# Performance work log

Hardware: AMD Instinct MI355X
Metric: run time of the kernel (lower is better)

Reference implementation:

```python
import jax, jax.numpy as jnp
import numpy as np
from jax import lax

F32 = jnp.float32
EDT_ITERS = 16  # iterations for erosion-based distance transform approximation


def _maxpool(x, win):
    # x: (B, 1, D, H, W); stride-1 'SAME' max pool (pads with -inf like torch)
    return lax.reduce_window(x, -jnp.inf, lax.max, (1, 1) + win, (1, 1, 1, 1, 1), 'SAME')


def _minpool(x, win):
    return -_maxpool(-x, win)


def soft_erode(img):
    p1 = _minpool(img, (3, 1, 1))
    p2 = _minpool(img, (1, 3, 1))
    p3 = _minpool(img, (1, 1, 3))
    return jnp.minimum(jnp.minimum(p1, p2), p3)


def soft_dilate(img):
    return _maxpool(img, (3, 3, 3))


def soft_open(img):
    return soft_dilate(soft_erode(img))


def soft_skel(img, num_iter=10):
    # clDice soft skeletonization (SoftSkeletonize, num_iter=10)
    skel = jax.nn.relu(img - soft_open(img))
    for _ in range(num_iter):
        img = soft_erode(img)
        delta = jax.nn.relu(img - soft_open(img))
        skel = skel + jax.nn.relu(delta - skel * delta)
    return skel


def edt_approx(mask):
    # mask: (B, D, H, W) binary float. Distance-to-background via iterated
    # 3x3x3 erosion (chessboard metric approximation of distance_transform_edt).
    m = mask[:, None]

    def body(carry, _):
        cur, acc = carry
        acc = acc + cur
        cur = _minpool(cur, (3, 3, 3))
        return (cur, acc), None

    (_, acc), _ = lax.scan(body, (m, jnp.zeros_like(m)), None, length=EDT_ITERS)
    return acc[:, 0]


def get_weights(mask_input, skel_input, prob_flag):
    # dim == 3 path of the original get_weights, vectorized over batch
    if prob_flag:
        mask = (mask_input > 0.5).astype(F32)
        skel = (skel_input > 0.5).astype(F32)
    else:
        mask, skel = mask_input, skel_input
    dist = lax.stop_gradient(edt_approx(mask)) * mask
    skel_radius = dist * skel
    red = (1, 2, 3)
    rmax = jnp.maximum(jnp.max(skel_radius, axis=red, keepdims=True), 1.0)
    rmin = jnp.maximum(jnp.min(skel_radius, axis=red, keepdims=True), 1.0)
    dist_map_norm = jnp.minimum(dist, rmax) / rmax
    skel_R_norm = skel_radius / rmax
    I_norm = ((rmax - skel_radius + rmin) / rmax) ** 2 * skel  # dim == 3 -> squared
    if prob_flag:
        return dist_map_norm * mask_input, skel_R_norm * mask_input, I_norm * skel_input
    return dist_map_norm * mask, skel_R_norm * mask, I_norm * skel


def binary_fg_prob(net_output):
    # max over foreground channels, 2-way softmax, foreground probability
    fore = jnp.max(net_output[:, 1:], axis=1, keepdims=True)
    logits2 = jnp.concatenate([net_output[:, :1], fore], axis=1)
    return jax.nn.softmax(logits2, axis=1)[:, 1]  # (B, D, H, W)


def general_union(pred, tgt, weight):
    smooth, alpha, eps = 1.0, 0.1, 1e-4
    inter = jnp.sum(weight * (pred + eps) ** 0.7 * tgt)
    union = jnp.sum(weight * (alpha * pred + (1.0 - alpha) * tgt))
    return 1.0 - (inter + smooth) / (union + smooth)


def union_loss(net_output, target):
    prob = binary_fg_prob(net_output)
    y_true = (target[:, 0] > 0).astype(F32)
    hard = lax.stop_gradient((prob > 0.5).astype(F32))
    skel_pred_hard = lax.stop_gradient(soft_skel(hard[:, None], 10)[:, 0])
    skel_true = lax.stop_gradient(soft_skel(y_true[:, None], 10)[:, 0])
    skel_pred_prob = skel_pred_hard * prob
    q_vl, _, q_sl = get_weights(y_true, skel_true, prob_flag=False)
    q_vp, _, q_sp = get_weights(prob, skel_pred_prob, prob_flag=True)
    return general_union(q_sp, q_vl, q_sp) + general_union(q_vp, q_sl, q_sl)


def cldice_loss(net_output, target, num_iter=10, smooth=1.0):
    prob = binary_fg_prob(net_output)
    y_true = (target[:, 0] > 0).astype(F32)
    skel_pred = soft_skel(prob[:, None], num_iter)[:, 0]
    skel_true = soft_skel(y_true[:, None], num_iter)[:, 0]
    tprec = (jnp.sum(skel_pred * y_true) + smooth) / (jnp.sum(skel_pred) + smooth)
    tsens = (jnp.sum(skel_true * prob) + smooth) / (jnp.sum(skel_true) + smooth)
    return 1.0 - 2.0 * tprec * tsens / (tprec + tsens)


def soft_dice_loss(net_output, target, smooth=1e-5):
    # nnUNet SoftDiceLoss: softmax nonlin, batch_dice=True, do_bg=False
    pred = jax.nn.softmax(net_output, axis=1)
    C = net_output.shape[1]
    onehot = jnp.moveaxis(jax.nn.one_hot(target[:, 0], C, dtype=F32), -1, 1)
    axes = (0, 2, 3, 4)
    tp = jnp.sum(pred * onehot, axis=axes)
    fp = jnp.sum(pred * (1.0 - onehot), axis=axes)
    fn = jnp.sum((1.0 - pred) * onehot, axis=axes)
    dc = (2.0 * tp + smooth) / (2.0 * tp + fp + fn + smooth)
    return -jnp.mean(dc[1:])


def ce_loss(net_output, labels):
    logp = jax.nn.log_softmax(net_output, axis=1)
    nll = -jnp.take_along_axis(logp, labels[:, None], axis=1)[:, 0]
    return jnp.mean(nll)


def _sobel_kernels():
    sx = np.array([[-1, 0, 1], [-2, 0, 2], [-1, 0, 1]], np.float32)
    kx_t = np.stack([sx, sx, sx], axis=0)[None, None]  # (1,1,3,3,3) OIDHW
    ky_t = np.transpose(kx_t, (0, 1, 3, 2, 4))
    kz_t = np.transpose(kx_t, (0, 1, 4, 2, 3))

    def pred_k(k):  # (1,2,3,3,3): second input channel is all-zero like the torch kernel
        return np.concatenate([k, np.zeros_like(k)], axis=1)

    return (pred_k(kx_t), pred_k(ky_t), pred_k(kz_t)), (kx_t, ky_t, kz_t)


def _conv3d(x, k):
    return lax.conv_general_dilated(x, jnp.asarray(k), (1, 1, 1), 'SAME',
                                    dimension_numbers=('NCDHW', 'OIDHW', 'NCDHW'))


def directional_loss(pred, target):
    kp, kt = _sobel_kernels()
    gp = jnp.stack([_conv3d(pred, k) for k in kp], axis=-1)    # (B,1,D,H,W,3)
    gt = jnp.stack([_conv3d(target, k) for k in kt], axis=-1)  # (B,1,D,H,W,3)

    def normalize(v):
        n = jnp.linalg.norm(v, axis=-1, keepdims=True)
        return v / jnp.maximum(n, 1e-12)

    gpn, gtn = normalize(gp), normalize(gt)
    num = jnp.sum(gpn * gtn, axis=-1)
    den = jnp.maximum(jnp.linalg.norm(gpn, axis=-1) * jnp.linalg.norm(gtn, axis=-1), 1e-8)
    return 1.0 - jnp.mean(num / den)


def connectivity_loss(pred, target):
    pb = (pred > 0.5).astype(F32)
    tb = (target > 0.5).astype(F32)
    return jnp.mean(jnp.abs(pb - tb))  # broadcasts (B,2,...) against (B,1,...)


def combined_loss(net_output, target):
    tgt_f = target.astype(F32)
    labels = target[:, 0]
    return (soft_dice_loss(net_output, target)
            + ce_loss(net_output, labels)
            + cldice_loss(net_output, target)
            + directional_loss(net_output, tgt_f)
            + connectivity_loss(net_output, tgt_f)
            + union_loss(net_output, target))


def setup_inputs() -> dict:
    key = jax.random.key(0)
    k1, k2 = jax.random.split(key)
    net_output = jax.random.normal(k1, (2, 2, 64, 128, 128), dtype=jnp.float32)
    target = jax.random.randint(k2, (2, 1, 64, 128, 128), 0, 2, dtype=jnp.int32)
    return {'net_output': net_output, 'target': target, 't_skeletonize_flage': 0}


def reference(net_output, target, t_skeletonize_flage):
    # t_skeletonize_flage=0 -> soft (morphological) skeletonization path
    return combined_loss(net_output, target)
```

## Files before the change

kernel.cpp:

```cpp
#include <hip/hip_runtime.h>
#include <math.h>

typedef unsigned long long u64;
typedef unsigned int u32;
typedef unsigned short u16;
typedef unsigned char u8;

#define VOL 1048576
#define NTOT 2097152
#define NWORDS 32768
#define PC0 2048
#define PC1 2048

union HU { u16 u; _Float16 h; };
__device__ __forceinline__ float h2f(u16 u){ HU x; x.u=u; return (float)x.h; }
__device__ __forceinline__ u16 f2h(float f){ HU x; x.h=(_Float16)f; return x.u; }
#define H_ONE2 0x3C003C00u

__device__ __forceinline__ u32 pmin(u32 a, u32 b){ u32 r; asm("v_pk_min_f16 %0, %1, %2" : "=v"(r) : "v"(a), "v"(b)); return r; }
__device__ __forceinline__ u32 pmax(u32 a, u32 b){ u32 r; asm("v_pk_max_f16 %0, %1, %2" : "=v"(r) : "v"(a), "v"(b)); return r; }

__device__ __forceinline__ double wred(double v){
  #pragma unroll
  for(int o=32;o;o>>=1) v += __shfl_down(v, o);
// ... 13 lines not shown
  u64 win;
  if (a<0)        win = w0 << (-a);
  else if (a==0)  win = w0;
  else if (a<64)  win = (w0>>a)|(w1<<(64-a));
  else            win = w1>>(a-64);
  if (x<31) win |= (1ull<<(31-x))-1;
  if (x>95) win |= (~0ull)<<(159-x);
  u64 inv = ~win;
  u64 tl = inv & 0xFFFFFFFFull;
  u64 tr = inv>>31;
  int dl = tl ? (31-(63-__clzll(tl))) : 99;
  int dr = tr ? (__ffsll((unsigned long long)tr)-1) : 99;
  return min(min(dl,dr),16);
}

__global__ __launch_bounds__(256) void k_init(const float* __restrict__ net, const int* __restrict__ tgt,
    u16* __restrict__ img, u16* __restrict__ prob, u64* __restrict__ ybits, u64* __restrict__ hbits,
    u64* __restrict__ bimg2, u8* __restrict__ dA, double* __restrict__ part)
{
  __shared__ u64 nyb[32], nhb[32];
  __shared__ u64 swy[16], swh[16];
  __shared__ double sw[5][4];
  int tid = threadIdx.x;
  int r = blockIdx.x*256 + tid;
  int n0 = r<<2;
  int b = n0>>20, v0 = n0&(VOL-1);
  const float* nb = net + (size_t)b*(2*VOL);
  float4 a0 = *(const float4*)&nb[v0];
  float4 a1 = *(const float4*)&nb[VOL+v0];
  int4  tv = *(const int4*)&tgt[n0];
  float x0a[4] = {a0.x,a0.y,a0.z,a0.w};
  float x1a[4] = {a1.x,a1.y,a1.z,a1.w};
  int   ta[4]  = {tv.x,tv.y,tv.z,tv.w};
  double ce=0,tp=0,spr=0,sy=0,conn=0;
  u32 pk[2] = {0,0};
  u32 y4=0, h4=0;
  #pragma unroll
  for(int e=0;e<4;e++){
    float d = x1a[e]-x0a[e];
    int yb = (ta[e]>0) ? 1 : 0;
    float p = 1.f/(1.f+__expf(-d));
    y4 |= (u32)yb<<e;
    h4 |= (u32)(d>0.f)<<e;
    pk[e>>1] |= (u32)f2h(p) << ((e&1)*16);
    ce += (double)(log1pf(__expf(-fabsf(d))) + fmaxf(yb? -d : d, 0.f));
    tp += (double)p*yb;
    spr += (double)p;
    sy += (double)yb;
    conn += (double)((int)((x0a[e]>0.5f)!=(yb!=0)) + (int)((x1a[e]>0.5f)!=(yb!=0)));
  }
  u32* f1 = (u32*)img;
  u32* f4 = (u32*)prob;
  int pi = r<<1;
  f1[pi] = pk[0]; f1[pi+1] = pk[1];
  f4[pi] = pk[0]; f4[pi+1] = pk[1];
  ((u8*)nyb)[tid] = (u8)y4;
  ((u8*)nhb)[tid] = (u8)h4;
  __syncthreads();
  if (tid < 16){
    u64 wy = (u64)nib_compact(nyb[tid*2]) | ((u64)nib_compact(nyb[tid*2+1])<<32);
    u64 wh = (u64)nib_compact(nhb[tid*2]) | ((u64)nib_compact(nhb[tid*2+1])<<32);
    int wi = blockIdx.x*16 + tid;
    ybits[wi]=wy; bimg2[wi]=wy;
    hbits[wi]=wh; bimg2[NWORDS+wi]=wh;
    swy[tid]=wy; swh[tid]=wh;
  }
  __syncthreads();
  {
    int ln = tid<<2;
    int row = ln>>7;
    int xq = ln&127;
    int gn0 = blockIdx.x*1024 + ln;
    u64 wy0 = swy[row*2], wy1 = swy[row*2+1];
    u64 wh0 = swh[row*2], wh1 = swh[row*2+1];
    u32 oy4=0, oh4=0;
    #pragma unroll
    for(int e=0;e<4;e++){
      oy4 |= (u32)edt_x1(wy0,wy1,xq+e) << (8*e);
      oh4 |= (u32)edt_x1(wh0,wh1,xq+e) << (8*e);
    }
    *(u32*)&dA[gn0] = oy4;
    *(u32*)&dA[(size_t)NTOT+gn0] = oh4;
  }
  int wid = tid>>6, lane = tid&63;
  double vals[5] = {ce,tp,spr,sy,conn};
  #pragma unroll
  for(int s=0;s<5;s++){ double rr = wred(vals[s]); if(lane==0) sw[s][wid]=rr; }
  __syncthreads();
  if(tid==0){
    #pragma unroll
    for(int s=0;s<5;s++) part[(size_t)s*PC0 + blockIdx.x] = sw[s][0]+sw[s][1]+sw[s][2]+sw[s][3];
  }
}

template<bool INIT>
__global__ __launch_bounds__(512) void fskel2(const u16* __restrict__ imgin, u16* __restrict__ imgout,
                                              u16* __restrict__ skel)
{
  __shared__ u32 A_[3920];
  __shared__ u32 B_[2592];
  __shared__ u32 C_[1800];
  int bid = blockIdx.x;
  int xb = bid&3, yb=(bid>>2)&15, zb=(bid>>6)&7, b=bid>>9;
  int X0=xb*32, Y0=yb*8, Z0=zb*8;
  const u32* vin = (const u32*)(imgin + (size_t)b*VOL);
  u32* vout = (u32*)(imgout + (size_t)b*VOL);
  u32* skl = (u32*)(skel + (size_t)b*VOL);
  int tid = threadIdx.x;

  for (int idx=tid; idx<3920; idx+=512){
    int z = idx/280; int rem = idx - z*280; int y = rem/20; int px = rem - y*20;
    int gz = Z0-3+z, gy = Y0-3+y, gx = X0-4+2*px;
    bool ok = ((unsigned)gz<64u) & ((unsigned)gy<128u) & ((unsigned)gx<128u);
    A_[idx] = ok ? vin[(gz<<13)+(gy<<6)+(gx>>1)] : H_ONE2;
  }
  __syncthreads();
  for (int idx=tid; idx<2592; idx+=512){
    int z = idx/216; int rem = idx - z*216; int y = rem/18; int px = rem - y*18;
    int gz = Z0-2+z, gy = Y0-2+y;
    bool zok = (unsigned)gz<64u, yok = (unsigned)gy<128u;
    bool xout = ((X0==0)&&(px==0)) || ((X0==96)&&(px==17));
    u32 v = H_ONE2;
    if (zok && yok && !xout){
      int c = (z+1)*280 + (y+1)*20 + (px+1);
      u32 C0=A_[c], L=A_[c-1], R=A_[c+1];
      u32 SL=(L>>16)|(C0<<16), SR=(C0>>16)|(R<<16);
      u32 m = pmin(pmin(SL,SR), C0);
      m = pmin(m, pmin(A_[c-20],A_[c+20]));
      v = pmin(m, pmin(A_[c-280],A_[c+280]));
    }
    B_[idx] = v;
  }
  __syncthreads();
  for (int idx=tid; idx<1800; idx+=512){
    int z = idx/180; int rem = idx - z*180; int y = rem/18; int px = rem - y*18;
    int gz = Z0-1+z, gy = Y0-1+y;
    bool zok=(unsigned)gz<64u, yok=(unsigned)gy<128u;
    bool xout = ((X0==0)&&(px==0)) || ((X0==96)&&(px==17));
    int pxm = (px>0)?px-1:0, pxp=(px<17)?px+1:17;
    u32 v = 0;
    if (zok && yok && !xout){
      int c = (z+1)*216 + (y+1)*18;
      u32 C0=B_[c+px], L=B_[c+pxm], R=B_[c+pxp];
      u32 SL=(L>>16)|(C0<<16), SR=(C0>>16)|(R<<16);
      u32 m = pmin(pmin(SL,SR), C0);
      m = pmin(m, pmin(B_[c+px-18],B_[c+px+18]));
      v = pmin(m, pmin(B_[c-216+px],B_[c+216+px]));
    }
    C_[idx] = v;
    if (px>=1 && px<=16 && y>=1 && y<=8 && z>=1 && z<=8)
      vout[(gz<<13)+(gy<<6)+((X0-2+2*px)>>1)] = v;
  }
  int zq = tid>>7, cc = tid&127;
  int oy = cc>>4, opx = cc&15;
  u32 ek0[2], ek1[2];
  #pragma unroll
  for(int j=0;j<2;j++){
    int z = zq*2+j;
    ek0[j] = A_[(z+3)*280 + (oy+3)*20 + (opx+2)];
    ek1[j] = B_[(z+2)*216 + (oy+2)*18 + (opx+1)];
  }
  __syncthreads();
  u32* X1 = A_; u32* X2 = A_ + 1600;
  for (int idx=tid; idx<3200; idx+=512){
    int arr = (idx>=1600);
    int r2 = arr ? idx-1600 : idx;
    int z = r2/160; int rem = r2 - z*160; int y = rem>>4; int px = rem&15;
    u32 v;
    if (!arr){
      int gz = Z0-1+z, gy = Y0-1+y;
      bool ok = ((unsigned)gz<64u) && ((unsigned)gy<128u);
      int c = (z+1)*216 + (y+1)*18 + (px+1);
      u32 C0=B_[c], L=B_[c-1], R=B_[c+1];
      if ((X0==0)&&(px==0)) L=0;
      if ((X0==96)&&(px==15)) R=0;
      u32 SL=(L>>16)|(C0<<16), SR=(C0>>16)|(R<<16);
      v = pmax(pmax(SL,SR), C0);
      if (!ok) v = 0;
    } else {
      int c = z*180 + y*18 + (px+1);
      u32 C0=C_[c], L=C_[c-1], R=C_[c+1];
      u32 SL=(L>>16)|(C0<<16), SR=(C0>>16)|(R<<16);
      v = pmax(pmax(SL,SR), C0);
    }
    A_[idx] = v;
  }
  __syncthreads();
  for (int idx=tid; idx<2560; idx+=512){
    int arr = (idx>=1280);
    int r2 = arr ? idx-1280 : idx;
    int z = r2>>7; int rem = r2&127; int y = rem>>4; int px = rem&15;
    const u32* Xs = arr ? X2 : X1;
    int c = z*160 + y*16 + px;
    B_[idx] = pmax(pmax(Xs[c], Xs[c+16]), Xs[c+32]);
  }
  __syncthreads();
  u32* Y1 = B_; u32* Y2 = B_ + 1280;
  {
    int gx = X0 + 2*opx;
    #pragma unroll
    for(int j=0;j<2;j++){
      int z = zq*2+j;
      int gz = Z0+z;
      int c = z*128 + oy*16 + opx;
      u32 o1 = pmax(pmax(Y1[c], Y1[c+128]), Y1[c+256]);
      u32 o2 = pmax(pmax(Y2[c], Y2[c+128]), Y2[c+256]);
      u32 idx = (u32)((gz<<13) + ((Y0+oy)<<6) + (gx>>1));
      float d0l = fmaxf(h2f((u16)ek0[j]) - h2f((u16)o1), 0.f);
      float d0h = fmaxf(h2f((u16)(ek0[j]>>16)) - h2f((u16)(o1>>16)), 0.f);
      float d1l = fmaxf(h2f((u16)ek1[j]) - h2f((u16)o2), 0.f);
      float d1h = fmaxf(h2f((u16)(ek1[j]>>16)) - h2f((u16)(o2>>16)), 0.f);
      float sl_, sh_;
      if (INIT){ sl_ = d0l; sh_ = d0h; }
      else {
        u32 swv = skl[idx];
        sl_ = h2f((u16)swv); sh_ = h2f((u16)(swv>>16));
        sl_ += fmaxf(d0l - sl_*d0l, 0.f); sh_ += fmaxf(d0h - sh_*d0h, 0.f);
      }
      sl_ += fmaxf(d1l - sl_*d1l, 0.f); sh_ += fmaxf(d1h - sh_*d1h, 0.f);
      skl[idx] = (u32)f2h(sl_) | ((u32)f2h(sh_)<<16);
    }
  }
}

__global__ __launch_bounds__(512) void fskel1(const u16* __restrict__ imgin, u16* __restrict__ skel)
{
  __shared__ u32 A2[2880];
  __shared__ u32 B2[1800];
  int bid = blockIdx.x;
  int xb = bid&3, yb=(bid>>2)&15, zb=(bid>>6)&7, b=bid>>9;
  int X0=xb*32, Y0=yb*8, Z0=zb*8;
  const u32* vin = (const u32*)(imgin + (size_t)b*VOL);
  u32* skl = (u32*)(skel + (size_t)b*VOL);
  int tid = threadIdx.x;
  for (int idx=tid; idx<2880; idx+=512){
    int z = idx/240; int rem = idx - z*240; int y = rem/20; int px = rem - y*20;
    int gz = Z0-2+z, gy = Y0-2+y, gx = X0-4+2*px;
    bool ok = ((unsigned)gz<64u) & ((unsigned)gy<128u) & ((unsigned)gx<128u);
    A2[idx] = ok ? vin[(gz<<13)+(gy<<6)+(gx>>1)] : H_ONE2;
  }
  __syncthreads();
  for (int idx=tid; idx<1800; idx+=512){
    int z = idx/180; int rem = idx - z*180; int y = rem/18; int px = rem - y*18;
    int gz = Z0-1+z, gy = Y0-1+y;
    bool zok=(unsigned)gz<64u, yok=(unsigned)gy<128u;
    bool xout = ((X0==0)&&(px==0)) || ((X0==96)&&(px==17));
    int pxm = (px>0)?px-1:0, pxp=(px<17)?px+1:17;
    u32 v = 0;
    if (zok && yok && !xout){
      int c = (z+1)*240 + (y+1)*20;
      u32 C0=A2[c+px+1], L=A2[c+pxm+1], R=A2[c+pxp+1];
      u32 SL=(L>>16)|(C0<<16), SR=(C0>>16)|(R<<16);
      u32 m = pmin(pmin(SL,SR), C0);
      m = pmin(m, pmin(A2[c+px+1-20],A2[c+px+1+20]));
      v = pmin(m, pmin(A2[c-240+px+1],A2[c+240+px+1]));
    }
    B2[idx] = v;
  }
  int zq = tid>>7, cc = tid&127;
  int oy = cc>>4, opx = cc&15;
  u32 ek[2];
  #pragma unroll
  for(int j=0;j<2;j++){
    int z = zq*2+j;
    ek[j] = A2[(z+2)*240 + (oy+2)*20 + (opx+2)];
  }
  __syncthreads();
  u32* X = A2;
  for (int idx=tid; idx<1600; idx+=512){
    int z = idx/160; int rem = idx - z*160; int y = rem>>4; int px = rem&15;
    int c = z*180 + y*18 + (px+1);
    u32 C0=B2[c], L=B2[c-1], R=B2[c+1];
    u32 SL=(L>>16)|(C0<<16), SR=(C0>>16)|(R<<16);
    A2[idx] = pmax(pmax(SL,SR), C0);
  }
  __syncthreads();
  u32* Y = B2;
  for (int idx=tid; idx<1280; idx+=512){
    int z = idx>>7; int rem = idx&127; int y = rem>>4; int px = rem&15;
    int c = z*160 + y*16 + px;
    B2[idx] = pmax(pmax(X[c], X[c+16]), X[c+32]);
  }
  __syncthreads();
  {
    int gx = X0 + 2*opx;
    #pragma unroll
    for(int j=0;j<2;j++){
      int z = zq*2+j;
      int gz = Z0+z;
      int c = z*128 + oy*16 + opx;
      u32 o = pmax(pmax(Y[c], Y[c+128]), Y[c+256]);
      u32 idx = (u32)((gz<<13) + ((Y0+oy)<<6) + (gx>>1));
      float dl = fmaxf(h2f((u16)ek[j]) - h2f((u16)o), 0.f);
      float dh = fmaxf(h2f((u16)(ek[j]>>16)) - h2f((u16)(o>>16)), 0.f);
      u32 swv = skl[idx];
      float sl_ = h2f((u16)swv), sh_ = h2f((u16)(swv>>16));
      sl_ += fmaxf(dl - sl_*dl, 0.f); sh_ += fmaxf(dh - sh_*dh, 0.f);
      skl[idx] = (u32)f2h(sl_) | ((u32)f2h(sh_)<<16);
    }
  }
}

__device__ __forceinline__ u64 berode_x(const u64* P, int tid){
  u64 c = P[tid];
  if (tid & 1) return c & ((c<<1)|(P[tid-1]>>63)) & ((c>>1)|(1ull<<63));
  else         return c & ((c<<1)|1ull) & ((c>>1)|(P[tid+1]<<63));
}
__device__ __forceinline__ u64 bdilate_x(const u64* P, int tid){
  u64 c = P[tid];
  if (tid & 1) return c | (c<<1) | (P[tid-1]>>63) | (c>>1);
  else         return c | (c<<1) | (c>>1) | (P[tid+1]<<63);
}

template<bool INIT>
__global__ __launch_bounds__(256) void bskel(const u64* __restrict__ imgin, u64* __restrict__ imgout,
                                             u64* __restrict__ skel)
{
  __shared__ u64 simg[4][256];
  __shared__ u64 se1[6][256];
  __shared__ u64 se2[2][256];
  __shared__ u64 sM[4][256];
  int bid = blockIdx.x;
  int tzb = bid & 31, b = (bid>>5)&1, m = bid>>6;
  int z0 = tzb*2, z1 = z0+2;
  size_t base = (size_t)m*NWORDS + (size_t)b*16384;
  const u64* vin = imgin + base;
  u64* vout = imgout + base;
  u64* skl = skel + base;
  int tid = threadIdx.x;
  int y = tid>>1;

  for (int s = z0-3; s <= z1+6; ++s){
    if (s <= z1+2)
      simg[(s+96)&3][tid] = ((unsigned)s<64u) ? vin[(s<<8)+tid] : ~0ull;
    { int t = s-2;
      if (t >= z0-2 && t <= z1+1){
        u64 r = ~0ull;
        if ((unsigned)t<64u){
          const u64* P = simg[(t+96)&3];
          if (INIT) r = P[tid];
          else {
            r = berode_x(P, tid);
            if(y>0)   r &= P[tid-2];
            if(y<127) r &= P[tid+2];
// ... 6 lines not shown
    { int t = s-4;
      if (t >= z0-1 && t <= z1){
        u64 r = 0;
        if ((unsigned)t<64u){
          const u64* P = se1[(t+96)%6];
          r = berode_x(P, tid);
          if(y>0)   r &= P[tid-2];
          if(y<127) r &= P[tid+2];
          r &= se1[(t-1+96)%6][tid] & se1[(t+1+96)%6][tid];
        }
        se2[(t+96)&1][tid] = r;
      }
    }
    { int t = s-5;
      if (t >= z0-1 && t <= z1){
        const u64* P = se2[(t+96)&1];
        u64 dm = bdilate_x(P, tid);
        if(y>0)   dm |= bdilate_x(P, tid-2);
        if(y<127) dm |= bdilate_x(P, tid+2);
        sM[(t+96)&3][tid] = dm;
      }
    }
    { int z = s-7;
      if (z >= z0 && z < z1){
        u64 open_ = sM[(z-1+96)&3][tid] | sM[(z+96)&3][tid] | sM[(z+1+96)&3][tid];
        u64 e1v = se1[(z+96)%6][tid];
        u64 d = e1v & ~open_;
        int gw = (z<<8)+tid;
        if (INIT) skl[gw] = d;
        else { skl[gw] |= d; vout[gw] = e1v; }
      }
    }
    __syncthreads();
  }
}

__global__ __launch_bounds__(256) void edt_py(const u8* __restrict__ din, u8* __restrict__ dout){
  int g = blockIdx.x*256 + threadIdx.x;
  int n = g & (NTOT-1);
  int c = (n >> 7) & 127;
  size_t idx = (size_t)g;
  int best = din[idx];
  #pragma unroll 4
  for (int k=1; k<=16; ++k){
    if (best <= k) break;
    int v = 255;
    if (c-k >= 0)   v = din[idx - (size_t)k*128];
    if (c+k < 128)  v = min(v, (int)din[idx + (size_t)k*128]);
    best = min(best, max(k, v));
  }
  dout[idx] = (u8)best;
}

__global__ __launch_bounds__(256) void edt_pz_part(const u8* __restrict__ din, u8* __restrict__ dout,
    const u64* __restrict__ skel2, const u64* __restrict__ hbits,
    u8* __restrict__ pmaxv, u8* __restrict__ pminv)
{
  int tid = threadIdx.x;
  int g = blockIdx.x*256 + tid;
  int m = g >> 21;
  int n = g & (NTOT-1);
  int c = (n >> 14) & 63;
  size_t idx = (size_t)g;
  int best = din[idx];
  #pragma unroll 4
  for (int k=1; k<=16; ++k){
// ... 93 lines not shown
    }
    wrow[tid] = wn;
  }
  __syncthreads();
  for (int idx=tid; idx<1920; idx+=256){
    int zr = idx/320; int rem = idx-zr*320; int yr = rem>>5; int x = rem&31;
    int c = zr*340 + yr*34 + x;
    float l0=lp[c], l1=lp[c+1], l2=lp[c+2];
    dxp[idx] = l2-l0;
    sxp[idx] = l0+2.f*l1+l2;
    u64 wn = wrow[zr*10+yr];
    int bm=(int)((wn>>x)&1ull), b1=(int)((wn>>(x+1))&1ull), bp=(int)((wn>>(x+2))&1ull);
    dxt8[idx] = (char)(bp-bm);
    sxt8[idx] = (u8)(bm+2*b1+bp);
  }
  __syncthreads();
  int oy = tid>>5, ox = tid&31;
  float A1[6],A2[6],A3[6];
  int   B1v[6],B2v[6],B3v[6];
  #pragma unroll
  for(int zr=0; zr<6; ++zr){
    int base = zr*320 + oy*32 + ox;
    float d0=dxp[base], d1=dxp[base+32], d2=dxp[base+64];
    A1[zr] = d0+2.f*d1+d2;
    A2[zr] = d0+d1+d2;
    float s0=sxp[base], s1=sxp[base+32], s2=sxp[base+64];
    A3[zr] = s0+s1+s2;
    int t0=dxt8[base], t1=dxt8[base+32], t2=dxt8[base+64];
    B1v[zr] = t0+2*t1+t2;
    B2v[zr] = t0+t1+t2;
    int u0=sxt8[base], u1=sxt8[base+32], u2=sxt8[base+64];
    B3v[zr] = u0+u1+u2;
  }
  double fsob=0,cl1=0,cl2=0,cl3=0,cl4=0,i1=0,un1=0,i2=0,un2=0;
  #pragma unroll
  for(int zc=0; zc<4; ++zc){
    float gpx = A1[zc]+A1[zc+1]+A1[zc+2];
    float gpy = A2[zc]+2.f*A2[zc+1]+A2[zc+2];
    float gpz = A3[zc+2]-A3[zc];
    float ftx = (float)(B1v[zc]+B1v[zc+1]+B1v[zc+2]);
    float fty = (float)(B2v[zc]+2*B2v[zc+1]+B2v[zc+2]);
    float ftz = (float)(B3v[zc+2]-B3v[zc]);
    float s1 = gpx*gpx+gpy*gpy+gpz*gpz;
    float s2 = ftx*ftx+fty*fty+ftz*ftz;
    if (s1>0.f && s2>0.f){
      float ip = rsqrtf(s1), it = rsqrtf(s2);
      fsob += (double)((gpx*ftx+gpy*fty+gpz*ftz)*ip*it);
    }
    int gz=Z0+zc, gy=Y0+oy, gx=X0+ox;
    int n = (b<<20)+(gz<<14)+(gy<<7)+gx;
    int yb = (int)((wrow[(zc+1)*10+(oy+1)] >> (ox+1)) & 1ull);
    int wi = n>>6, bit = n&63;
    int hd = (int)((hbits[wi]>>bit)&1ull);
    int sT = (int)((skel2[wi]>>bit)&1ull);
    int sH = (int)((skel2[NWORDS+wi]>>bit)&1ull);
    float dT = (float)acc[n];
    float dH = (float)acc[(size_t)NTOT+n];
    float p  = h2f(prob[n]);
    float sk = h2f(skelp[n]);
    cl1 += (double)(sk*(float)yb);
    cl2 += (double)sk;
    float q_vl = yb ? fminf(dT,rmaxT)/rmaxT : 0.f;
    if (sT){
      cl3 += (double)p; cl4 += 1.0;
      float t=(rmaxT-dT+rminT)/rmaxT; float q_sl=t*t;
      float q_vp = fminf(dH,rmaxH)/rmaxH*p;
      i2  += (double)(q_sl*__powf(q_vp+1e-4f,0.7f)*q_sl);
      un2 += (double)(q_sl*(0.1f*q_vp+0.9f*q_sl));
    }
    if (sH & hd){
      float t=(rmaxH-dH+rminH)/rmaxH; float q_sp=t*t*p;
      i1  += (double)(q_sp*__powf(q_sp+1e-4f,0.7f)*q_vl);
      un1 += (double)(q_sp*(0.1f*q_sp+0.9f*q_vl));
    }
  }
  int wid = tid>>6, lane = tid&63;
  double vals[9] = {fsob,cl1,cl2,cl3,cl4,i1,un1,i2,un2};
  #pragma unroll
  for(int s=0;s<9;s++){ double rr = wred(vals[s]); if(lane==0) sw[s][wid]=rr; }
  __syncthreads();
  if(tid==0){
    #pragma unroll
    for(int s=0;s<9;s++) part1[(size_t)s*PC1 + bid] = sw[s][0]+sw[s][1]+sw[s][2]+sw[s][3];
  }
}

__global__ __launch_bounds__(256) void k_reduce_mid(const double* __restrict__ part0,
                                                    const double* __restrict__ part1,
                                                    double* __restrict__ tot){
  int s = blockIdx.x;
  const double* src; int n;
  if (s < 5){ src = part0 + (size_t)s*PC0; n = PC0; }
  else      { src = part1 + (size_t)(s-5)*PC1; n = PC1; }
  double v=0;
  for(int i=threadIdx.x;i<n;i+=256) v += src[i];
  __shared__ double sd[256];
  sd[threadIdx.x]=v; __syncthreads();
  for(int k=128;k>0;k>>=1){ if((int)threadIdx.x<k) sd[threadIdx.x]+=sd[threadIdx.x+k]; __syncthreads(); }
  if(threadIdx.x==0) tot[s]=sd[0];
}

__global__ void k_fin(const double* __restrict__ tot, float* __restrict__ out){
  if(threadIdx.x==0 && blockIdx.x==0){
    const double N = (double)NTOT;
    double ce = tot[0]/N;
    double tp=tot[1], fp=tot[2]-tot[1], fn=tot[3]-tot[1];
    double dice = -((2.0*tp+1e-5)/(2.0*tp+fp+fn+1e-5));
    double conn = tot[4]/(2.0*N);
    double dir  = 1.0 - tot[5]/N;
    double tprec = (tot[6]+1.0)/(tot[7]+1.0);
// ... 6 lines not shown
}

extern "C" void kernel_launch(void* const* d_in, const int* in_sizes, int n_in,
                              void* d_out, int out_size, void* d_ws, size_t ws_size,
                              hipStream_t stream)
{
  (void)in_sizes; (void)n_in; (void)out_size; (void)ws_size;
  const float* net = (const float*)d_in[0];
  const int*   tgt = (const int*)d_in[1];
  float* out = (float*)d_out;
  char* w = (char*)d_ws;
  const size_t MB = 1024*1024;
  u16* F1 = (u16*)(w + 0*MB);
  u16* F2 = (u16*)(w + 4*MB);
  u16* F3 = (u16*)(w + 8*MB);
  u16* F4 = (u16*)(w + 12*MB);
  u64* ybits = (u64*)(w + 16*MB);
  u64* hbits = ybits + NWORDS;
  u64* skel2 = hbits + NWORDS;
  u64* bping = skel2 + 2*NWORDS;
  u64* bpong = bping + 2*NWORDS;
  u8*  dA    = (u8*)(bpong + 2*NWORDS);
  u8*  dB    = dA + (size_t)2*NTOT;
  double* part0 = (double*)(dB + (size_t)2*NTOT);
  double* part1 = part0 + (size_t)5*PC0;
  double* tot   = part1 + (size_t)9*PC1;
  u8* pmaxv = (u8*)(tot + 16);
  u8* pminv = pmaxv + 16384;
  u32* mm  = (u32*)(pminv + 16384);

  k_init<<<PC0, 256, 0, stream>>>(net, tgt, F1, F4, ybits, hbits, bping, dA, part0);

  bskel<true><<<128,256,0,stream>>>(bping, bpong, skel2);
  {
    u64* pi=bping; u64* po=bpong;
    for(int i=0;i<10;i++){ bskel<false><<<128,256,0,stream>>>(pi,po,skel2); u64* t=pi; pi=po; po=t; }
  }

  fskel2<true><<<1024,512,0,stream>>>(F1, F3, F2);
  fskel2<false><<<1024,512,0,stream>>>(F3, F1, F2);
  fskel2<false><<<1024,512,0,stream>>>(F1, F3, F2);
  fskel2<false><<<1024,512,0,stream>>>(F3, F1, F2);
  fskel2<false><<<1024,512,0,stream>>>(F1, F3, F2);
  fskel1<<<1024,512,0,stream>>>(F3, F2);

  const int GE = (2*NTOT)/256;
  edt_py<<<GE,256,0,stream>>>(dA, dB);
  edt_pz_part<<<GE,256,0,stream>>>(dB, dA, skel2, hbits, pmaxv, pminv);
  rmm2<<<1,256,0,stream>>>(pmaxv, pminv, mm);

  k_tail<<<PC1,256,0,stream>>>(net, F4, F2, ybits, hbits, skel2, dA, mm, part1);
  k_reduce_mid<<<14,256,0,stream>>>(part0, part1, tot);
  k_fin<<<1,64,0,stream>>>(tot, out);
}
```

Baseline: 303.2 us.

## Fuse binary skeleton iterations into float skeleton kernels as extra blocks

Six of the ten binary-skeleton iterations now run as 128 extra blocks appended to each float soft-skeleton launch, in a combined fsk_b kernel that dispatches on block index. The binary work uses a z-streaming erode/open pipeline over bit-packed words, so six small, poorly occupied launches disappear and that work overlaps with the float tiles. Per-thread loss accumulators in k_init and k_tail also switch from double to float, with double kept only for the cross-lane reduction. This trades some accumulation precision and a larger shared-memory footprint per block for fewer launches and fewer fp64 operations.

```diff
diff --git a/kernel.cpp b/kernel.cpp
--- a/kernel.cpp
+++ b/kernel.cpp
@@ -69,7 +69,7 @@
   float x0a[4] = {a0.x,a0.y,a0.z,a0.w};
   float x1a[4] = {a1.x,a1.y,a1.z,a1.w};
   int   ta[4]  = {tv.x,tv.y,tv.z,tv.w};
-  double ce=0,tp=0,spr=0,sy=0,conn=0;
+  float ce=0,tp=0,spr=0,sy=0,conn=0;
   u32 pk[2] = {0,0};
   u32 y4=0, h4=0;
   #pragma unroll
@@ -80,11 +80,11 @@
     y4 |= (u32)yb<<e;
     h4 |= (u32)(d>0.f)<<e;
     pk[e>>1] |= (u32)f2h(p) << ((e&1)*16);
-    ce += (double)(log1pf(__expf(-fabsf(d))) + fmaxf(yb? -d : d, 0.f));
-    tp += (double)p*yb;
-    spr += (double)p;
-    sy += (double)yb;
-    conn += (double)((int)((x0a[e]>0.5f)!=(yb!=0)) + (int)((x1a[e]>0.5f)!=(yb!=0)));
+    ce += log1pf(__expf(-fabsf(d))) + fmaxf(yb? -d : d, 0.f);
+    tp += p*(float)yb;
+    spr += p;
+    sy += (float)yb;
+    conn += (float)((int)((x0a[e]>0.5f)!=(yb!=0)) + (int)((x1a[e]>0.5f)!=(yb!=0)));
   }
   u32* f1 = (u32*)img;
   u32* f4 = (u32*)prob;
@@ -120,7 +120,7 @@
     *(u32*)&dA[(size_t)NTOT+gn0] = oh4;
   }
   int wid = tid>>6, lane = tid&63;
-  double vals[5] = {ce,tp,spr,sy,conn};
+  double vals[5] = {(double)ce,(double)tp,(double)spr,(double)sy,(double)conn};
   #pragma unroll
   for(int s=0;s<5;s++){ double rr = wred(vals[s]); if(lane==0) sw[s][wid]=rr; }
   __syncthreads();
@@ -130,223 +130,15 @@
   }
 }
 
-template<bool INIT>
-__global__ __launch_bounds__(512) void fskel2(const u16* __restrict__ imgin, u16* __restrict__ imgout,
-                                              u16* __restrict__ skel)
-{
-  __shared__ u32 A_[3920];
-  __shared__ u32 B_[2592];
-  __shared__ u32 C_[1800];
-  int bid = blockIdx.x;
-  int xb = bid&3, yb=(bid>>2)&15, zb=(bid>>6)&7, b=bid>>9;
-  int X0=xb*32, Y0=yb*8, Z0=zb*8;
-  const u32* vin = (const u32*)(imgin + (size_t)b*VOL);
-  u32* vout = (u32*)(imgout + (size_t)b*VOL);
-  u32* skl = (u32*)(skel + (size_t)b*VOL);
-  int tid = threadIdx.x;
-
-  for (int idx=tid; idx<3920; idx+=512){
-    int z = idx/280; int rem = idx - z*280; int y = rem/20; int px = rem - y*20;
-    int gz = Z0-3+z, gy = Y0-3+y, gx = X0-4+2*px;
-    bool ok = ((unsigned)gz<64u) & ((unsigned)gy<128u) & ((unsigned)gx<128u);
-    A_[idx] = ok ? vin[(gz<<13)+(gy<<6)+(gx>>1)] : H_ONE2;
-  }
-  __syncthreads();
-  for (int idx=tid; idx<2592; idx+=512){
-    int z = idx/216; int rem = idx - z*216; int y = rem/18; int px = rem - y*18;
-    int gz = Z0-2+z, gy = Y0-2+y;
-    bool zok = (unsigned)gz<64u, yok = (unsigned)gy<128u;
-    bool xout = ((X0==0)&&(px==0)) || ((X0==96)&&(px==17));
-    u32 v = H_ONE2;
-    if (zok && yok && !xout){
-      int c = (z+1)*280 + (y+1)*20 + (px+1);
-      u32 C0=A_[c], L=A_[c-1], R=A_[c+1];
-      u32 SL=(L>>16)|(C0<<16), SR=(C0>>16)|(R<<16);
-      u32 m = pmin(pmin(SL,SR), C0);
-      m = pmin(m, pmin(A_[c-20],A_[c+20]));
-      v = pmin(m, pmin(A_[c-280],A_[c+280]));
-    }
-    B_[idx] = v;
-  }
-  __syncthreads();
-  for (int idx=tid; idx<1800; idx+=512){
-    int z = idx/180; int rem = idx - z*180; int y = rem/18; int px = rem - y*18;
-    int gz = Z0-1+z, gy = Y0-1+y;
-    bool zok=(unsigned)gz<64u, yok=(unsigned)gy<128u;
-    bool xout = ((X0==0)&&(px==0)) || ((X0==96)&&(px==17));
-    int pxm = (px>0)?px-1:0, pxp=(px<17)?px+1:17;
-    u32 v = 0;
-    if (zok && yok && !xout){
-      int c = (z+1)*216 + (y+1)*18;
-      u32 C0=B_[c+px], L=B_[c+pxm], R=B_[c+pxp];
-      u32 SL=(L>>16)|(C0<<16), SR=(C0>>16)|(R<<16);
-      u32 m = pmin(pmin(SL,SR), C0);
-      m = pmin(m, pmin(B_[c+px-18],B_[c+px+18]));
-      v = pmin(m, pmin(B_[c-216+px],B_[c+216+px]));
-    }
-    C_[idx] = v;
-    if (px>=1 && px<=16 && y>=1 && y<=8 && z>=1 && z<=8)
-      vout[(gz<<13)+(gy<<6)+((X0-2+2*px)>>1)] = v;
-  }
-  int zq = tid>>7, cc = tid&127;
-  int oy = cc>>4, opx = cc&15;
-  u32 ek0[2], ek1[2];
-  #pragma unroll
-  for(int j=0;j<2;j++){
-    int z = zq*2+j;
-    ek0[j] = A_[(z+3)*280 + (oy+3)*20 + (opx+2)];
-    ek1[j] = B_[(z+2)*216 + (oy+2)*18 + (opx+1)];
-  }
-  __syncthreads();
-  u32* X1 = A_; u32* X2 = A_ + 1600;
-  for (int idx=tid; idx<3200; idx+=512){
-    int arr = (idx>=1600);
-    int r2 = arr ? idx-1600 : idx;
-    int z = r2/160; int rem = r2 - z*160; int y = rem>>4; int px = rem&15;
-    u32 v;
-    if (!arr){
-      int gz = Z0-1+z, gy = Y0-1+y;
-      bool ok = ((unsigned)gz<64u) && ((unsigned)gy<128u);
-      int c = (z+1)*216 + (y+1)*18 + (px+1);
-      u32 C0=B_[c], L=B_[c-1], R=B_[c+1];
-      if ((X0==0)&&(px==0)) L=0;
-      if ((X0==96)&&(px==15)) R=0;
-      u32 SL=(L>>16)|(C0<<16), SR=(C0>>16)|(R<<16);
-      v = pmax(pmax(SL,SR), C0);
-      if (!ok) v = 0;
-    } else {
-      int c = z*180 + y*18 + (px+1);
-      u32 C0=C_[c], L=C_[c-1], R=C_[c+1];
-      u32 SL=(L>>16)|(C0<<16), SR=(C0>>16)|(R<<16);
-      v = pmax(pmax(SL,SR), C0);
-    }
-    A_[idx] = v;
-  }
-  __syncthreads();
-  for (int idx=tid; idx<2560; idx+=512){
-    int arr = (idx>=1280);
-    int r2 = arr ? idx-1280 : idx;
-    int z = r2>>7; int rem = r2&127; int y = rem>>4; int px = rem&15;
-    const u32* Xs = arr ? X2 : X1;
-    int c = z*160 + y*16 + px;
-    B_[idx] = pmax(pmax(Xs[c], Xs[c+16]), Xs[c+32]);
-  }
-  __syncthreads();
-  u32* Y1 = B_; u32* Y2 = B_ + 1280;
-  {
-    int gx = X0 + 2*opx;
-    #pragma unroll
-    for(int j=0;j<2;j++){
-      int z = zq*2+j;
-      int gz = Z0+z;
-      int c = z*128 + oy*16 + opx;
-      u32 o1 = pmax(pmax(Y1[c], Y1[c+128]), Y1[c+256]);
-      u32 o2 = pmax(pmax(Y2[c], Y2[c+128]), Y2[c+256]);
-      u32 idx = (u32)((gz<<13) + ((Y0+oy)<<6) + (gx>>1));
-      float d0l = fmaxf(h2f((u16)ek0[j]) - h2f((u16)o1), 0.f);
-      float d0h = fmaxf(h2f((u16)(ek0[j]>>16)) - h2f((u16)(o1>>16)), 0.f);
-      float d1l = fmaxf(h2f((u16)ek1[j]) - h2f((u16)o2), 0.f);
-      float d1h = fmaxf(h2f((u16)(ek1[j]>>16)) - h2f((u16)(o2>>16)), 0.f);
-      float sl_, sh_;
-      if (INIT){ sl_ = d0l; sh_ = d0h; }
-      else {
-        u32 swv = skl[idx];
-        sl_ = h2f((u16)swv); sh_ = h2f((u16)(swv>>16));
-        sl_ += fmaxf(d0l - sl_*d0l, 0.f); sh_ += fmaxf(d0h - sh_*d0h, 0.f);
-      }
-      sl_ += fmaxf(d1l - sl_*d1l, 0.f); sh_ += fmaxf(d1h - sh_*d1h, 0.f);
-      skl[idx] = (u32)f2h(sl_) | ((u32)f2h(sh_)<<16);
-    }
-  }
-}
-
-__global__ __launch_bounds__(512) void fskel1(const u16* __restrict__ imgin, u16* __restrict__ skel)
-{
-  __shared__ u32 A2[2880];
-  __shared__ u32 B2[1800];
-  int bid = blockIdx.x;
-  int xb = bid&3, yb=(bid>>2)&15, zb=(bid>>6)&7, b=bid>>9;
-  int X0=xb*32, Y0=yb*8, Z0=zb*8;
-  const u32* vin = (const u32*)(imgin + (size_t)b*VOL);
-  u32* skl = (u32*)(skel + (size_t)b*VOL);
-  int tid = threadIdx.x;
-  for (int idx=tid; idx<2880; idx+=512){
-    int z = idx/240; int rem = idx - z*240; int y = rem/20; int px = rem - y*20;
-    int gz = Z0-2+z, gy = Y0-2+y, gx = X0-4+2*px;
-    bool ok = ((unsigned)gz<64u) & ((unsigned)gy<128u) & ((unsigned)gx<128u);
-    A2[idx] = ok ? vin[(gz<<13)+(gy<<6)+(gx>>1)] : H_ONE2;
-  }
-  __syncthreads();
-  for (int idx=tid; idx<1800; idx+=512){
-    int z = idx/180; int rem = idx - z*180; int y = rem/18; int px = rem - y*18;
-    int gz = Z0-1+z, gy = Y0-1+y;
-    bool zok=(unsigned)gz<64u, yok=(unsigned)gy<128u;
-    bool xout = ((X0==0)&&(px==0)) || ((X0==96)&&(px==17));
-    int pxm = (px>0)?px-1:0, pxp=(px<17)?px+1:17;
-    u32 v = 0;
-    if (zok && yok && !xout){
-      int c = (z+1)*240 + (y+1)*20;
-      u32 C0=A2[c+px+1], L=A2[c+pxm+1], R=A2[c+pxp+1];
-      u32 SL=(L>>16)|(C0<<16), SR=(C0>>16)|(R<<16);
-      u32 m = pmin(pmin(SL,SR), C0);
-      m = pmin(m, pmin(A2[c+px+1-20],A2[c+px+1+20]));
-      v = pmin(m, pmin(A2[c-240+px+1],A2[c+240+px+1]));
-    }
-    B2[idx] = v;
-  }
-  int zq = tid>>7, cc = tid&127;
-  int oy = cc>>4, opx = cc&15;
-  u32 ek[2];
-  #pragma unroll
-  for(int j=0;j<2;j++){
-    int z = zq*2+j;
-    ek[j] = A2[(z+2)*240 + (oy+2)*20 + (opx+2)];
-  }
-  __syncthreads();
-  u32* X = A2;
-  for (int idx=tid; idx<1600; idx+=512){
-    int z = idx/160; int rem = idx - z*160; int y = rem>>4; int px = rem&15;
-    int c = z*180 + y*18 + (px+1);
-    u32 C0=B2[c], L=B2[c-1], R=B2[c+1];
-    u32 SL=(L>>16)|(C0<<16), SR=(C0>>16)|(R<<16);
-    A2[idx] = pmax(pmax(SL,SR), C0);
-  }
-  __syncthreads();
-  u32* Y = B2;
-  for (int idx=tid; idx<1280; idx+=512){
-    int z = idx>>7; int rem = idx&127; int y = rem>>4; int px = rem&15;
-    int c = z*160 + y*16 + px;
-    B2[idx] = pmax(pmax(X[c], X[c+16]), X[c+32]);
-  }
-  __syncthreads();
-  {
-    int gx = X0 + 2*opx;
-    #pragma unroll
-    for(int j=0;j<2;j++){
-      int z = zq*2+j;
-      int gz = Z0+z;
-      int c = z*128 + oy*16 + opx;
-      u32 o = pmax(pmax(Y[c], Y[c+128]), Y[c+256]);
-      u32 idx = (u32)((gz<<13) + ((Y0+oy)<<6) + (gx>>1));
-      float dl = fmaxf(h2f((u16)ek[j]) - h2f((u16)o), 0.f);
-      float dh = fmaxf(h2f((u16)(ek[j]>>16)) - h2f((u16)(o>>16)), 0.f);
-      u32 swv = skl[idx];
-      float sl_ = h2f((u16)swv), sh_ = h2f((u16)(swv>>16));
-      sl_ += fmaxf(dl - sl_*dl, 0.f); sh_ += fmaxf(dh - sh_*dh, 0.f);
-      skl[idx] = (u32)f2h(sl_) | ((u32)f2h(sh_)<<16);
-    }
-  }
-}
-
-__device__ __forceinline__ u64 berode_x(const u64* P, int tid){
-  u64 c = P[tid];
-  if (tid & 1) return c & ((c<<1)|(P[tid-1]>>63)) & ((c>>1)|(1ull<<63));
-  else         return c & ((c<<1)|1ull) & ((c>>1)|(P[tid+1]<<63));
-}
-__device__ __forceinline__ u64 bdilate_x(const u64* P, int tid){
-  u64 c = P[tid];
-  if (tid & 1) return c | (c<<1) | (P[tid-1]>>63) | (c>>1);
-  else         return c | (c<<1) | (c>>1) | (P[tid+1]<<63);
+__device__ __forceinline__ u64 berode_x(const u64* P, int t){
+  u64 c = P[t];
+  if (t & 1) return c & ((c<<1)|(P[t-1]>>63)) & ((c>>1)|(1ull<<63));
+  else       return c & ((c<<1)|1ull) & ((c>>1)|(P[t+1]<<63));
+}
+__device__ __forceinline__ u64 bdilate_x(const u64* P, int t){
+  u64 c = P[t];
+  if (t & 1) return c | (c<<1) | (P[t-1]>>63) | (c>>1);
+  else       return c | (c<<1) | (c>>1) | (P[t+1]<<63);
 }
 
 template<bool INIT>
@@ -419,6 +211,275 @@
       }
     }
     __syncthreads();
+  }
+}
+
+template<int MODE>
+__global__ __launch_bounds__(512) void fsk_b(
+    const u16* __restrict__ imgin, u16* __restrict__ imgout, u16* __restrict__ skel,
+    const u64* __restrict__ bin, u64* __restrict__ bout, u64* __restrict__ bskl)
+{
+  __shared__ __align__(16) char smem_[33280];
+  int bid = blockIdx.x;
+  int tid = threadIdx.x;
+  if (bid < 1024){
+    int xb = bid&3, yb=(bid>>2)&15, zb=(bid>>6)&7, b=bid>>9;
+    int X0=xb*32, Y0=yb*8, Z0=zb*8;
+    const u32* vin = (const u32*)(imgin + (size_t)b*VOL);
+    u32* skl = (u32*)(skel + (size_t)b*VOL);
+    if (MODE < 2){
+      u32* A_ = (u32*)smem_;
+      u32* B_ = A_ + 3920;
+      u32* C_ = B_ + 2592;
+      u32* vout = (u32*)(imgout + (size_t)b*VOL);
+      for (int idx=tid; idx<3920; idx+=512){
+        int z = idx/280; int rem = idx - z*280; int y = rem/20; int px = rem - y*20;
+        int gz = Z0-3+z, gy = Y0-3+y, gx = X0-4+2*px;
+        bool ok = ((unsigned)gz<64u) & ((unsigned)gy<128u) & ((unsigned)gx<128u);
+        A_[idx] = ok ? vin[(gz<<13)+(gy<<6)+(gx>>1)] : H_ONE2;
+      }
+      __syncthreads();
+      for (int idx=tid; idx<2592; idx+=512){
+        int z = idx/216; int rem = idx - z*216; int y = rem/18; int px = rem - y*18;
+        int gz = Z0-2+z, gy = Y0-2+y;
+        bool zok = (unsigned)gz<64u, yok = (unsigned)gy<128u;
+        bool xout = ((X0==0)&&(px==0)) || ((X0==96)&&(px==17));
+        u32 v = H_ONE2;
+        if (zok && yok && !xout){
+          int c = (z+1)*280 + (y+1)*20 + (px+1);
+          u32 C0=A_[c], L=A_[c-1], R=A_[c+1];
+          u32 SL=(L>>16)|(C0<<16), SR=(C0>>16)|(R<<16);
+          u32 m = pmin(pmin(SL,SR), C0);
+          m = pmin(m, pmin(A_[c-20],A_[c+20]));
+          v = pmin(m, pmin(A_[c-280],A_[c+280]));
+        }
+        B_[idx] = v;
+      }
+      __syncthreads();
+      for (int idx=tid; idx<1800; idx+=512){
+        int z = idx/180; int rem = idx - z*180; int y = rem/18; int px = rem - y*18;
+        int gz = Z0-1+z, gy = Y0-1+y;
+        bool zok=(unsigned)gz<64u, yok=(unsigned)gy<128u;
+        bool xout = ((X0==0)&&(px==0)) || ((X0==96)&&(px==17));
+        int pxm = (px>0)?px-1:0, pxp=(px<17)?px+1:17;
+        u32 v = 0;
+        if (zok && yok && !xout){
+          int c = (z+1)*216 + (y+1)*18;
+          u32 C0=B_[c+px], L=B_[c+pxm], R=B_[c+pxp];
+          u32 SL=(L>>16)|(C0<<16), SR=(C0>>16)|(R<<16);
+          u32 m = pmin(pmin(SL,SR), C0);
+          m = pmin(m, pmin(B_[c+px-18],B_[c+px+18]));
+          v = pmin(m, pmin(B_[c-216+px],B_[c+216+px]));
+        }
+        C_[idx] = v;
+        if (px>=1 && px<=16 && y>=1 && y<=8 && z>=1 && z<=8)
+          vout[(gz<<13)+(gy<<6)+((X0-2+2*px)>>1)] = v;
+      }
+      int zq = tid>>7, cc = tid&127;
+      int oy = cc>>4, opx = cc&15;
+      u32 ek0[2], ek1[2];
+      #pragma unroll
+      for(int j=0;j<2;j++){
+        int z = zq*2+j;
+        ek0[j] = A_[(z+3)*280 + (oy+3)*20 + (opx+2)];
+        ek1[j] = B_[(z+2)*216 + (oy+2)*18 + (opx+1)];
+      }
+      __syncthreads();
+      u32* X1 = A_; u32* X2 = A_ + 1600;
+      for (int idx=tid; idx<3200; idx+=512){
+        int arr = (idx>=1600);
+        int r2 = arr ? idx-1600 : idx;
+        int z = r2/160; int rem = r2 - z*160; int y = rem>>4; int px = rem&15;
+        u32 v;
+        if (!arr){
+          int gz = Z0-1+z, gy = Y0-1+y;
+          bool ok = ((unsigned)gz<64u) && ((unsigned)gy<128u);
+          int c = (z+1)*216 + (y+1)*18 + (px+1);
+          u32 C0=B_[c], L=B_[c-1], R=B_[c+1];
+          if ((X0==0)&&(px==0)) L=0;
+          if ((X0==96)&&(px==15)) R=0;
+          u32 SL=(L>>16)|(C0<<16), SR=(C0>>16)|(R<<16);
+          v = pmax(pmax(SL,SR), C0);
+          if (!ok) v = 0;
+        } else {
+          int c = z*180 + y*18 + (px+1);
+          u32 C0=C_[c], L=C_[c-1], R=C_[c+1];
+          u32 SL=(L>>16)|(C0<<16), SR=(C0>>16)|(R<<16);
+          v = pmax(pmax(SL,SR), C0);
+        }
+        A_[idx] = v;
+      }
+      __syncthreads();
+      for (int idx=tid; idx<2560; idx+=512){
+        int arr = (idx>=1280);
+        int r2 = arr ? idx-1280 : idx;
+        int z = r2>>7; int rem = r2&127; int y = rem>>4; int px = rem&15;
+        const u32* Xs = arr ? X2 : X1;
+        int c = z*160 + y*16 + px;
+        B_[idx] = pmax(pmax(Xs[c], Xs[c+16]), Xs[c+32]);
+      }
+      __syncthreads();
+      u32* Y1 = B_; u32* Y2 = B_ + 1280;
+      {
+        int gx = X0 + 2*opx;
+        #pragma unroll
+        for(int j=0;j<2;j++){
+          int z = zq*2+j;
+          int gz = Z0+z;
+          int c = z*128 + oy*16 + opx;
+          u32 o1 = pmax(pmax(Y1[c], Y1[c+128]), Y1[c+256]);
+          u32 o2 = pmax(pmax(Y2[c], Y2[c+128]), Y2[c+256]);
+          u32 idx = (u32)((gz<<13) + ((Y0+oy)<<6) + (gx>>1));
+          float d0l = fmaxf(h2f((u16)ek0[j]) - h2f((u16)o1), 0.f);
+          float d0h = fmaxf(h2f((u16)(ek0[j]>>16)) - h2f((u16)(o1>>16)), 0.f);
+          float d1l = fmaxf(h2f((u16)ek1[j]) - h2f((u16)o2), 0.f);
+          float d1h = fmaxf(h2f((u16)(ek1[j]>>16)) - h2f((u16)(o2>>16)), 0.f);
+          float sl_, sh_;
+          if (MODE==0){ sl_ = d0l; sh_ = d0h; }
+          else {
+            u32 swv = skl[idx];
+            sl_ = h2f((u16)swv); sh_ = h2f((u16)(swv>>16));
+            sl_ += fmaxf(d0l - sl_*d0l, 0.f); sh_ += fmaxf(d0h - sh_*d0h, 0.f);
+          }
+          sl_ += fmaxf(d1l - sl_*d1l, 0.f); sh_ += fmaxf(d1h - sh_*d1h, 0.f);
+          skl[idx] = (u32)f2h(sl_) | ((u32)f2h(sh_)<<16);
+        }
+      }
+    } else {
+      u32* A2 = (u32*)smem_;
+      u32* B2 = A2 + 2880;
+      for (int idx=tid; idx<2880; idx+=512){
+        int z = idx/240; int rem = idx - z*240; int y = rem/20; int px = rem - y*20;
+        int gz = Z0-2+z, gy = Y0-2+y, gx = X0-4+2*px;
+        bool ok = ((unsigned)gz<64u) & ((unsigned)gy<128u) & ((unsigned)gx<128u);
+        A2[idx] = ok ? vin[(gz<<13)+(gy<<6)+(gx>>1)] : H_ONE2;
+      }
+      __syncthreads();
+      for (int idx=tid; idx<1800; idx+=512){
+        int z = idx/180; int rem = idx - z*180; int y = rem/18; int px = rem - y*18;
+        int gz = Z0-1+z, gy = Y0-1+y;
+        bool zok=(unsigned)gz<64u, yok=(unsigned)gy<128u;
+        bool xout = ((X0==0)&&(px==0)) || ((X0==96)&&(px==17));
+        int pxm = (px>0)?px-1:0, pxp=(px<17)?px+1:17;
+        u32 v = 0;
+        if (zok && yok && !xout){
+          int c = (z+1)*240 + (y+1)*20;
+          u32 C0=A2[c+px+1], L=A2[c+pxm+1], R=A2[c+pxp+1];
+          u32 SL=(L>>16)|(C0<<16), SR=(C0>>16)|(R<<16);
+          u32 m = pmin(pmin(SL,SR), C0);
+          m = pmin(m, pmin(A2[c+px+1-20],A2[c+px+1+20]));
+          v = pmin(m, pmin(A2[c-240+px+1],A2[c+240+px+1]));
+        }
+        B2[idx] = v;
+      }
+      int zq = tid>>7, cc = tid&127;
+      int oy = cc>>4, opx = cc&15;
+      u32 ek[2];
+      #pragma unroll
+      for(int j=0;j<2;j++){
+        int z = zq*2+j;
+        ek[j] = A2[(z+2)*240 + (oy+2)*20 + (opx+2)];
+      }
+      __syncthreads();
+      u32* X = A2;
+      for (int idx=tid; idx<1600; idx+=512){
+        int z = idx/160; int rem = idx - z*160; int y = rem>>4; int px = rem&15;
+        int c = z*180 + y*18 + (px+1);
+        u32 C0=B2[c], L=B2[c-1], R=B2[c+1];
+        u32 SL=(L>>16)|(C0<<16), SR=(C0>>16)|(R<<16);
+        A2[idx] = pmax(pmax(SL,SR), C0);
+      }
+      __syncthreads();
+      u32* Y = B2;
+      for (int idx=tid; idx<1280; idx+=512){
+        int z = idx>>7; int rem = idx&127; int y = rem>>4; int px = rem&15;
+        int c = z*160 + y*16 + px;
+        B2[idx] = pmax(pmax(X[c], X[c+16]), X[c+32]);
+      }
+      __syncthreads();
+      {
+        int gx = X0 + 2*opx;
+        #pragma unroll
+        for(int j=0;j<2;j++){
+          int z = zq*2+j;
+          int gz = Z0+z;
+          int c = z*128 + oy*16 + opx;
+          u32 o = pmax(pmax(Y[c], Y[c+128]), Y[c+256]);
+          u32 idx = (u32)((gz<<13) + ((Y0+oy)<<6) + (gx>>1));
+          float dl = fmaxf(h2f((u16)ek[j]) - h2f((u16)o), 0.f);
+          float dh = fmaxf(h2f((u16)(ek[j]>>16)) - h2f((u16)(o>>16)), 0.f);
+          u32 swv = skl[idx];
+          float sl_ = h2f((u16)swv), sh_ = h2f((u16)(swv>>16));
+          sl_ += fmaxf(dl - sl_*dl, 0.f); sh_ += fmaxf(dh - sh_*dh, 0.f);
+          skl[idx] = (u32)f2h(sl_) | ((u32)f2h(sh_)<<16);
+        }
+      }
+    }
+  } else {
+    u64* sim = (u64*)smem_;
+    u64* se1 = sim + 1024;
+    u64* se2 = se1 + 1536;
+    u64* sM  = se2 + 512;
+    int bid2 = bid - 1024;
+    int tzb = bid2 & 31, b = (bid2>>5)&1, m = bid2>>6;
+    int z0 = tzb*2, z1 = z0+2;
+    size_t base = (size_t)m*NWORDS + (size_t)b*16384;
+    const u64* vin = bin + base;
+    u64* vout = bout + base;
+    u64* skl = bskl + base;
+    int y = tid>>1;
+    for (int s = z0-3; s <= z1+6; ++s){
+      if (tid < 256){
+        if (s <= z1+2)
+          sim[((s+96)&3)*256+tid] = ((unsigned)s<64u) ? vin[(s<<8)+tid] : ~0ull;
+        { int t = s-2;
+          if (t >= z0-2 && t <= z1+1){
+            u64 r = ~0ull;
+            if ((unsigned)t<64u){
+              const u64* P = sim + ((t+96)&3)*256;
+              r = berode_x(P, tid);
+              if(y>0)   r &= P[tid-2];
+              if(y<127) r &= P[tid+2];
+              r &= sim[((t-1+96)&3)*256+tid] & sim[((t+1+96)&3)*256+tid];
+            }
+            se1[((t+96)%6)*256+tid] = r;
+          }
+        }
+        { int t = s-4;
+          if (t >= z0-1 && t <= z1){
+            u64 r = 0;
+            if ((unsigned)t<64u){
+              const u64* P = se1 + ((t+96)%6)*256;
+              r = berode_x(P, tid);
+              if(y>0)   r &= P[tid-2];
+              if(y<127) r &= P[tid+2];
+              r &= se1[((t-1+96)%6)*256+tid] & se1[((t+1+96)%6)*256+tid];
+            }
+            se2[((t+96)&1)*256+tid] = r;
+          }
+        }
+        { int t = s-5;
+          if (t >= z0-1 && t <= z1){
+            const u64* P = se2 + ((t+96)&1)*256;
+            u64 dm = bdilate_x(P, tid);
+            if(y>0)   dm |= bdilate_x(P, tid-2);
+            if(y<127) dm |= bdilate_x(P, tid+2);
+            sM[((t+96)&3)*256+tid] = dm;
+          }
+        }
+        { int z = s-7;
+          if (z >= z0 && z < z1){
+            u64 open_ = sM[((z-1+96)&3)*256+tid] | sM[((z+96)&3)*256+tid] | sM[((z+1+96)&3)*256+tid];
+            u64 e1v = se1[((z+96)%6)*256+tid];
+            u64 d = e1v & ~open_;
+            int gw = (z<<8)+tid;
+            skl[gw] |= d;
+            vout[gw] = e1v;
+          }
+        }
+      }
+      __syncthreads();
+    }
   }
 }
 
@@ -578,7 +639,7 @@
     int u0=sxt8[base], u1=sxt8[base+32], u2=sxt8[base+64];
     B3v[zr] = u0+u1+u2;
   }
-  double fsob=0,cl1=0,cl2=0,cl3=0,cl4=0,i1=0,un1=0,i2=0,un2=0;
+  float fsob=0,cl1=0,cl2=0,cl3=0,cl4=0,i1=0,un1=0,i2=0,un2=0;
   #pragma unroll
   for(int zc=0; zc<4; ++zc){
     float gpx = A1[zc]+A1[zc+1]+A1[zc+2];
@@ -591,7 +652,7 @@
     float s2 = ftx*ftx+fty*fty+ftz*ftz;
     if (s1>0.f && s2>0.f){
       float ip = rsqrtf(s1), it = rsqrtf(s2);
-      fsob += (double)((gpx*ftx+gpy*fty+gpz*ftz)*ip*it);
+      fsob += (gpx*ftx+gpy*fty+gpz*ftz)*ip*it;
     }
     int gz=Z0+zc, gy=Y0+oy, gx=X0+ox;
     int n = (b<<20)+(gz<<14)+(gy<<7)+gx;
@@ -604,24 +665,25 @@
     float dH = (float)acc[(size_t)NTOT+n];
     float p  = h2f(prob[n]);
     float sk = h2f(skelp[n]);
-    cl1 += (double)(sk*(float)yb);
-    cl2 += (double)sk;
+    cl1 += sk*(float)yb;
+    cl2 += sk;
     float q_vl = yb ? fminf(dT,rmaxT)/rmaxT : 0.f;
     if (sT){
-      cl3 += (double)p; cl4 += 1.0;
+      cl3 += p; cl4 += 1.f;
       float t=(rmaxT-dT+rminT)/rmaxT; float q_sl=t*t;
       float q_vp = fminf(dH,rmaxH)/rmaxH*p;
-      i2  += (double)(q_sl*__powf(q_vp+1e-4f,0.7f)*q_sl);
-      un2 += (double)(q_sl*(0.1f*q_vp+0.9f*q_sl));
+      i2  += q_sl*__powf(q_vp+1e-4f,0.7f)*q_sl;
+      un2 += q_sl*(0.1f*q_vp+0.9f*q_sl);
     }
     if (sH & hd){
       float t=(rmaxH-dH+rminH)/rmaxH; float q_sp=t*t*p;
-      i1  += (double)(q_sp*__powf(q_sp+1e-4f,0.7f)*q_vl);
-      un1 += (double)(q_sp*(0.1f*q_sp+0.9f*q_vl));
+      i1  += q_sp*__powf(q_sp+1e-4f,0.7f)*q_vl;
+      un1 += q_sp*(0.1f*q_sp+0.9f*q_vl);
     }
   }
   int wid = tid>>6, lane = tid&63;
-  double vals[9] = {fsob,cl1,cl2,cl3,cl4,i1,un1,i2,un2};
+  double vals[9] = {(double)fsob,(double)cl1,(double)cl2,(double)cl3,(double)cl4,
+                    (double)i1,(double)un1,(double)i2,(double)un2};
   #pragma unroll
   for(int s=0;s<9;s++){ double rr = wred(vals[s]); if(lane==0) sw[s][wid]=rr; }
   __syncthreads();
@@ -694,17 +756,17 @@
   k_init<<<PC0, 256, 0, stream>>>(net, tgt, F1, F4, ybits, hbits, bping, dA, part0);
 
   bskel<true><<<128,256,0,stream>>>(bping, bpong, skel2);
-  {
-    u64* pi=bping; u64* po=bpong;
-    for(int i=0;i<10;i++){ bskel<false><<<128,256,0,stream>>>(pi,po,skel2); u64* t=pi; pi=po; po=t; }
-  }
-
-  fskel2<true><<<1024,512,0,stream>>>(F1, F3, F2);
-  fskel2<false><<<1024,512,0,stream>>>(F3, F1, F2);
-  fskel2<false><<<1024,512,0,stream>>>(F1, F3, F2);
-  fskel2<false><<<1024,512,0,stream>>>(F3, F1, F2);
-  fskel2<false><<<1024,512,0,stream>>>(F1, F3, F2);
-  fskel1<<<1024,512,0,stream>>>(F3, F2);
+  bskel<false><<<128,256,0,stream>>>(bping, bpong, skel2);
+  bskel<false><<<128,256,0,stream>>>(bpong, bping, skel2);
+  bskel<false><<<128,256,0,stream>>>(bping, bpong, skel2);
+  bskel<false><<<128,256,0,stream>>>(bpong, bping, skel2);
+
+  fsk_b<0><<<1152,512,0,stream>>>(F1, F3, F2, bping, bpong, skel2);
+  fsk_b<1><<<1152,512,0,stream>>>(F3, F1, F2, bpong, bping, skel2);
+  fsk_b<1><<<1152,512,0,stream>>>(F1, F3, F2, bping, bpong, skel2);
+  fsk_b<1><<<1152,512,0,stream>>>(F3, F1, F2, bpong, bping, skel2);
+  fsk_b<1><<<1152,512,0,stream>>>(F1, F3, F2, bping, bpong, skel2);
+  fsk_b<2><<<1152,512,0,stream>>>(F3, F1, F2, bpong, bping, skel2);
 
   const int GE = (2*NTOT)/256;
   edt_py<<<GE,256,0,stream>>>(dA, dB);
```

Result: faster. 271.3 us (median of 2 runs) (-10.5%).
